# Kernel optimization log

Hardware: AMD Instinct MI355X
Metric: run time of the kernel (lower is better)

The kernel has to match this reference:

```python
import jax, jax.numpy as jnp
import numpy as np

R = 5            # num_relations
NEG_SLOPE = 0.2
N1 = 30000       # layer0 target count
N2 = 15000       # layer1 target count


def brgcn_conv(x_src, x_tgt, edge_index, edge_type, Wj, Wi, att_j, att_i,
               Wq, Wk, Wv, sw, sb, Wrel, heads, outc):
    """One BRGCNConv layer: per-relation GAT edge softmax + bilevel relation attention."""
    N = x_tgt.shape[0]
    hc = heads * outc
    hj = (x_src @ Wj).reshape(-1, heads, outc)   # [Ns,H,C]
    hi = (x_tgt @ Wi).reshape(-1, heads, outc)   # [N,H,C]
    src, tgt = edge_index[0], edge_index[1]
    xj = hj[src]                                  # [E,H,C]
    xi = hi[tgt]                                  # [E,H,C]
    # relation-specific attention logits per edge
    aj = jnp.sum(att_j[edge_type] * xj, axis=-1)  # [E,H]
    ai = jnp.sum(att_i[edge_type] * xi, axis=-1)  # [E,H]
    alpha = jax.nn.leaky_relu(aj + ai, NEG_SLOPE)
    # edge softmax grouped by (target node, relation) == per-relation propagate
    seg = tgt * R + edge_type                     # [E]
    nseg = N * R
    amax = jax.ops.segment_max(alpha, seg, num_segments=nseg)
    amax = jnp.where(jnp.isfinite(amax), amax, 0.0)
    ex = jnp.exp(alpha - amax[seg])
    den = jax.ops.segment_sum(ex, seg, num_segments=nseg)
    w = ex / jnp.maximum(den[seg], 1e-16)         # [E,H]
    msg = (w[:, :, None] * xj).reshape(-1, hc)    # [E,H*C]
    z = jax.ops.segment_sum(msg, seg, num_segments=nseg)
    z = z.reshape(N, R, hc).transpose(1, 0, 2)    # [R,N,H*C]; zero rows where no edges
    # per-relation Q/K/V
    q = jnp.einsum('rnd,rde->rne', z, Wq).reshape(R, N, heads, outc)
    k = jnp.einsum('rnd,rde->rne', z, Wk).reshape(R, N, heads, outc)
    v = jnp.einsum('rnd,rde->rne', z, Wv).reshape(R, N, heads, outc)
    # bilevel relation attention: psi[r,s,n,h] = <q_r, k_s>
    psi = jnp.einsum('rnhc,snhc->rsnh', q, k)
    mask = (psi == 0) & (jnp.sum(psi, axis=1, keepdims=True) != 0)
    prob = jax.nn.softmax(jnp.where(mask, -jnp.inf, psi), axis=1)
    delta = jnp.einsum('rsnh,snhc->rnhc', prob, v).reshape(R, N, hc)
    out = jnp.einsum('rnd,r->nd', delta, Wrel[:, 0])
    # single node type -> node_self[0] applied to every target node
    return out + x_tgt @ sw + sb


def setup_inputs() -> dict:
    key = jax.random.key(0)
    ks = jax.random.split(key, 32)
    H0, C0, H1, C1 = 4, 64, 1, 40
    IN, HC0 = 128, H0 * C0
    NG, N0 = 200000, 100000
    E0, E1 = 300000, 150000
    f = lambda k, s: jax.random.normal(k, s, dtype=jnp.float32) * 0.05
    return dict(
        n_id=jax.random.randint(ks[1], (N0,), 0, NG),
        local_node_idx=jax.random.randint(ks[2], (NG,), 0, NG),
        node_type=jnp.zeros((NG,), dtype=jnp.int32),
        edge_index0=jax.random.randint(ks[3], (2, E0), 0, N1),
        edge_type0=jax.random.randint(ks[4], (E0,), 0, R),
        edge_index1=jax.random.randint(ks[5], (2, E1), 0, N2),
        edge_type1=jax.random.randint(ks[6], (E1,), 0, R),
        emb=f(ks[0], (NG, IN)),
        Wj0=f(ks[7], (IN, HC0)), Wi0=f(ks[8], (IN, HC0)),
        att_j0=f(ks[9], (R, H0, C0)), att_i0=f(ks[10], (R, H0, C0)),
        Wq0=f(ks[11], (R, HC0, HC0)), Wk0=f(ks[12], (R, HC0, HC0)), Wv0=f(ks[13], (R, HC0, HC0)),
        sw0=f(ks[14], (IN, HC0)), sb0=f(ks[15], (HC0,)), Wrel0=f(ks[16], (R, 1)),
        Wj1=f(ks[17], (HC0, C1)), Wi1=f(ks[18], (HC0, C1)),
        att_j1=f(ks[19], (R, H1, C1)), att_i1=f(ks[20], (R, H1, C1)),
        Wq1=f(ks[21], (R, C1, C1)), Wk1=f(ks[22], (R, C1, C1)), Wv1=f(ks[23], (R, C1, C1)),
        sw1=f(ks[24], (HC0, C1)), sb1=f(ks[25], (C1,)), Wrel1=f(ks[26], (R, 1)),
    )


def reference(n_id, local_node_idx, node_type, edge_index0, edge_type0,
              edge_index1, edge_type1, emb,
              Wj0, Wi0, att_j0, att_i0, Wq0, Wk0, Wv0, sw0, sb0, Wrel0,
              Wj1, Wi1, att_j1, att_i1, Wq1, Wk1, Wv1, sw1, sb1, Wrel1):
    # group_input: single node type, all features from the embedding table
    x = emb[local_node_idx[n_id]]
    x1 = brgcn_conv(x, x[:N1], edge_index0, edge_type0, Wj0, Wi0, att_j0, att_i0,
                    Wq0, Wk0, Wv0, sw0, sb0, Wrel0, heads=4, outc=64)
    x1 = jax.nn.relu(x1)  # dropout p=0 in eval
    x2 = brgcn_conv(x1, x1[:N2], edge_index1, edge_type1, Wj1, Wi1, att_j1, att_i1,
                    Wq1, Wk1, Wv1, sw1, sb1, Wrel1, heads=1, outc=40)
    return jax.nn.log_softmax(x2, axis=-1)
```

## Files before the change

### kernel.cpp

```cpp
#include <hip/hip_runtime.h>
#include <hip/hip_bf16.h>

#define DI __device__ __forceinline__

DI float b2f(unsigned short u) {
    union { unsigned int i; float f; } x; x.i = ((unsigned int)u) << 16; return x.f;
}
DI unsigned short f2b(float f) {
    union { float f; unsigned int i; } x; x.f = f;
    unsigned int r = x.i + 0x7fff + ((x.i >> 16) & 1);
    return (unsigned short)(r >> 16);
}
DI float ldin(const void* p, long i, int f32) {
    return f32 ? ((const float*)p)[i] : b2f(((const unsigned short*)p)[i]);
}
DI void stval(float* p, float v) { *p = v; }
DI void stval(unsigned short* p, float v) { *p = f2b(v); }

static constexpr int N1 = 30000, N2 = 15000, R = 5;
static constexpr int IN = 128, HC0 = 256, C1 = 40;
static constexpr float NEGBIG = -1e30f;
static constexpr int LDK = 64;

typedef short bf16x8 __attribute__((ext_vector_type(8)));
typedef float f32x4 __attribute__((ext_vector_type(4)));

__global__ void detect_k(const void* emb, int* flag)
{
    int lane = threadIdx.x;
    int bad = 0;
    for (int j = 0; j < 4; ++j) {
        float f = b2f(((const unsigned short*)emb)[lane * 4 + j]);
        if (!(fabsf(f) < 1e8f)) bad = 1;
    }
    unsigned long long anybad = __ballot(bad != 0);
    if (lane == 0) *flag = (anybad != 0ull) ? 1 : 0;
}

struct PrepJobs {
    const void* src[12];
    unsigned short* dst[12];
    int K[12];
    int N[12];
    int per[12];
};
__global__ __launch_bounds__(256) void prep_all_k(
    PrepJobs J,
    const void* aj0, const void* ai0, const void* aj1, const void* ai1,
    unsigned short* A0j, unsigned short* A0i, unsigned short* A1j, unsigned short* A1i,
    int* __restrict__ cnt, int cntn,
    const int* __restrict__ dflag)
{
    const int f32 = *dflag;
    const int y = blockIdx.y;
    long t = (long)blockIdx.x * 256 + threadIdx.x;
    if (y < 12) {
        if (t >= J.per[y]) return;
        const int K = J.K[y], N = J.N[y];
        long kn = (long)K * N;
        long b = t / kn, rem = t % kn;
        long k = rem / N, n = rem % N;
        J.dst[y][(b * N + n) * K + k] = f2b(ldin(J.src[y], t, f32));
    } else {
        if (t < 20 * 256) {
            int j = (int)(t >> 8), k = (int)(t & 255);
            int h = j & 3, r = j >> 2;
            bool on = (k >> 6) == h;
            A0j[t] = f2b(on ? ldin(aj0, r * 256 + k, f32) : 0.f);
            A0i[t] = f2b(on ? ldin(ai0, r * 256 + k, f32) : 0.f);
        }
        if (t < 5 * 40) {
            A1j[t] = f2b(ldin(aj1, t, f32));
            A1i[t] = f2b(ldin(ai1, t, f32));
        }
        if (t < cntn) cnt[t] = 0;
    }
}

__global__ __launch_bounds__(256) void gather_k(
    const int* __restrict__ n_id, const int* __restrict__ lidx,
    const void* __restrict__ emb, unsigned short* __restrict__ x, int rows,
    const int* __restrict__ dflag)
{
    const int f32 = *dflag;
    long t = (long)blockIdx.x * 256 + threadIdx.x;
    long n = t >> 7, d = t & 127;
    if (n >= rows) return;
    long row = lidx[n_id[n]];
    x[n * IN + d] = f2b(ldin(emb, row * IN + d, f32));
}

DI void stage_fast(const unsigned short* __restrict__ G, int K,
                   unsigned short* S, int wave, int lane)
{
    const int p = lane >> 3;
    const int scol = ((lane & 7) ^ p) * 8;
#pragma unroll
    for (int t = 0; t < 4; ++t) {
        int row = t * 32 + wave * 8 + p;
        const unsigned short* src = G + (long)row * K + scol;
        unsigned short* dst = S + (t * 32 + wave * 8) * LDK;
        __builtin_amdgcn_global_load_lds(
            (const __attribute__((address_space(1))) unsigned int*)src,
            (__attribute__((address_space(3))) unsigned int*)dst, 16, 0, 0);
    }
}
DI void stage_slow(const unsigned short* __restrict__ G, int rows, int K,
                   int r0, int k0, unsigned short* S, int tid)
{
    const int sr = tid >> 1, sq = (tid & 1) * 32;
    const int sx = sr & 7;
    unsigned short* drow = S + sr * LDK;
    const unsigned short* g = G + (long)(r0 + sr) * K + k0 + sq;
    const bool rowok = (r0 + sr) < rows;
    const int s0 = sq >> 3;
    if (rowok && (k0 + sq + 32) <= K) {
        const uint4* gv = (const uint4*)g;
        uint4 a = gv[0], b = gv[1], c = gv[2], d = gv[3];
        *(uint4*)(drow + (((s0 + 0) ^ sx) << 3)) = a;
        *(uint4*)(drow + (((s0 + 1) ^ sx) << 3)) = b;
        *(uint4*)(drow + (((s0 + 2) ^ sx) << 3)) = c;
        *(uint4*)(drow + (((s0 + 3) ^ sx) << 3)) = d;
    } else if (!rowok) {
        uint4 zz = {0u, 0u, 0u, 0u};
        *(uint4*)(drow + (((s0 + 0) ^ sx) << 3)) = zz;
        *(uint4*)(drow + (((s0 + 1) ^ sx) << 3)) = zz;
        *(uint4*)(drow + (((s0 + 2) ^ sx) << 3)) = zz;
        *(uint4*)(drow + (((s0 + 3) ^ sx) << 3)) = zz;
    } else {
#pragma unroll 8
        for (int j = 0; j < 32; ++j) {
            int col = sq + j;
            int k = k0 + col;
            int widx = (((col >> 3) ^ sx) << 3) | (col & 7);
            drow[widx] = (k < K) ? g[j] : (unsigned short)0;
        }
    }
}

template <typename OT>
DI void gemm_mfma_body(
    const unsigned short* __restrict__ A, const unsigned short* __restrict__ Bt,
    OT* __restrict__ C, const void* __restrict__ bias, int f32,
    int M, int N, int K, unsigned short* As, unsigned short* Bs)
{
    const int tid = threadIdx.x;
    const int m0 = blockIdx.y * 128, n0 = blockIdx.x * 128;
    const int lane = tid & 63, wave = tid >> 6;
    const int wm = (wave & 1) * 64, wn = (wave >> 1) * 64;
    const int row16 = lane & 15, quad = lane >> 4;
    const bool kfull = (K & 63) == 0;
    const bool fastA = kfull && (m0 + 128 <= M);
    const bool fastB = kfull && (n0 + 128 <= N);
    f32x4 acc[4][4];
#pragma unroll
    for (int i = 0; i < 4; ++i)
#pragma unroll
        for (int j = 0; j < 4; ++j) acc[i][j] = {0.f, 0.f, 0.f, 0.f};

    for (int k0 = 0; k0 < K; k0 += 64) {
        if (fastA) stage_fast(A + (long)m0 * K + k0, K, As, wave, lane);
        else       stage_slow(A, M, K, m0, k0, As, tid);
        if (fastB) stage_fast(Bt + (long)n0 * K + k0, K, Bs, wave, lane);
        else       stage_slow(Bt, N, K, n0, k0, Bs, tid);
        __syncthreads();
#pragma unroll
        for (int ks = 0; ks < 64; ks += 32) {
            const int sw = (((quad + (ks >> 3)) ^ (row16 & 7)) << 3);
            bf16x8 af[4], bfr[4];
#pragma unroll
            for (int i = 0; i < 4; ++i)
                af[i] = *(const bf16x8*)(As + (wm + i * 16 + row16) * LDK + sw);
#pragma unroll
            for (int j = 0; j < 4; ++j)
                bfr[j] = *(const bf16x8*)(Bs + (wn + j * 16 + row16) * LDK + sw);
#pragma unroll
            for (int i = 0; i < 4; ++i)
#pragma unroll
                for (int j = 0; j < 4; ++j)
                    acc[i][j] = __builtin_amdgcn_mfma_f32_16x16x32_bf16(
                        af[i], bfr[j], acc[i][j], 0, 0, 0);
        }
        __syncthreads();
    }
#pragma unroll
    for (int i = 0; i < 4; ++i) {
#pragma unroll
        for (int reg = 0; reg < 4; ++reg) {
            const int gr = m0 + wm + i * 16 + quad * 4 + reg;
            if (gr >= M) continue;
#pragma unroll
            for (int j = 0; j < 4; ++j) {
                const int gc = n0 + wn + j * 16 + row16;
                if (gc >= N) continue;
                float v = acc[i][j][reg];
                if (bias) v += ldin(bias, gc, f32);
                stval(&C[(long)gr * N + gc], v);
            }
        }
    }
}

template <typename OT>
__global__ __launch_bounds__(256) void gemm_mfma3_k(
    const unsigned short* A0, const unsigned short* A1, const unsigned short* A2,
    const unsigned short* Bt0, const unsigned short* Bt1, const unsigned short* Bt2,
    OT* C0, OT* C1, OT* C2,
    const void* bias0, const void* bias1, const void* bias2,
    const int* __restrict__ dflag,
    int M, int N, int K, long sA, long sB, long sC, int nbatch)
{
    __shared__ unsigned short As[128 * LDK];
    __shared__ unsigned short Bs[128 * LDK];
    const int f32 = *dflag;
    const int sel = blockIdx.z / nbatch, b = blockIdx.z % nbatch;
    const unsigned short* A  = (sel == 0 ? A0 : sel == 1 ? A1 : A2) + (long)b * sA;
    const unsigned short* Bt = (sel == 0 ? Bt0 : sel == 1 ? Bt1 : Bt2) + (long)b * sB;
    OT* C = (sel == 0 ? C0 : sel == 1 ? C1 : C2) + (long)b * sC;
    const void* bias = sel == 0 ? bias0 : sel == 1 ? bias1 : bias2;
    gemm_mfma_body<OT>(A, Bt, C, bias, f32, M, N, K, As, Bs);
}

__global__ __launch_bounds__(256) void hist_k(const int* __restrict__ ei, int E, int* __restrict__ cnt)
{
    int e = blockIdx.x * 256 + threadIdx.x;
    if (e < E) atomicAdd(&cnt[ei[E + e]], 1);
}
__global__ __launch_bounds__(256) void scan1_k(
    const int* __restrict__ cnt, int* __restrict__ off, int* __restrict__ bsum, int n)
{
    __shared__ int buf[256];
    int i = blockIdx.x * 256 + threadIdx.x;
    int v = (i < n) ? cnt[i] : 0;
    buf[threadIdx.x] = v;
    __syncthreads();
#pragma unroll
    for (int s = 1; s < 256; s <<= 1) {
        int t = (threadIdx.x >= s) ? buf[threadIdx.x - s] : 0;
        __syncthreads();
        buf[threadIdx.x] += t;
        __syncthreads();
    }
    if (i < n) off[i] = buf[threadIdx.x] - v;
    if (threadIdx.x == 255) bsum[blockIdx.x] = buf[255];
}
__global__ void scan2_k(int* __restrict__ bsum, int nb, int* __restrict__ total_dst)
{
    __shared__ int buf[256];
    int v = (threadIdx.x < nb) ? bsum[threadIdx.x] : 0;
    buf[threadIdx.x] = v;
    __syncthreads();
#pragma unroll
    for (int s = 1; s < 256; s <<= 1) {
        int t = (threadIdx.x >= s) ? buf[threadIdx.x - s] : 0;
        __syncthreads();
        buf[threadIdx.x] += t;
        __syncthreads();
    }
    if (threadIdx.x < nb) bsum[threadIdx.x] = buf[threadIdx.x] - v;
    if (threadIdx.x == 255) *total_dst = buf[255];
}
__global__ __launch_bounds__(256) void scan3_k(
    int* __restrict__ off, int* __restrict__ cursor, const int* __restrict__ bsum,
    int* __restrict__ cnt, int n)
{
    int i = blockIdx.x * 256 + threadIdx.x;
    if (i < n) {
        int v = off[i] + bsum[blockIdx.x];
        off[i] = v;
        cursor[i] = v;
        cnt[i] = 0;
    }
}

__global__ __launch_bounds__(256) void scatter0_k(
    const int* __restrict__ ei, const int* __restrict__ et, int E,
    int* __restrict__ cursor,
    const float* __restrict__ ajn, const float* __restrict__ ain,
    int* __restrict__ src_s, int* __restrict__ rt_s, float* __restrict__ w4_s)
{
    int e = blockIdx.x * 256 + threadIdx.x;
    if (e >= E) return;
    int src = ei[e], tgt = ei[E + e], r = et[e];
    int p = atomicAdd(&cursor[tgt], 1);
    src_s[p] = src; rt_s[p] = r;
    float4 a = *(const float4*)(ajn + (long)src * 20 + r * 4);
    float4 b = *(const float4*)(ain + (long)tgt * 20 + r * 4);
    float4 w;
    float s0 = a.x + b.x, s1 = a.y + b.y, s2 = a.z + b.z, s3 = a.w + b.w;
    s0 = s0 > 0.f ? s0 : 0.2f * s0;  s1 = s1 > 0.f ? s1 : 0.2f * s1;
    s2 = s2 > 0.f ? s2 : 0.2f * s2;  s3 = s3 > 0.f ? s3 : 0.2f * s3;
    w.x = expf(fminf(s0, 60.f)); w.y = expf(fminf(s1, 60.f));
    w.z = expf(fminf(s2, 60.f)); w.w = expf(fminf(s3, 60.f));
    *(float4*)(w4_s + (long)p * 4) = w;
}
__global__ __launch_bounds__(256) void scatter1_k(
    const int* __restrict__ ei, const int* __restrict__ et, int E,
    int* __restrict__ cursor,
    const float* __restrict__ ajn, const float* __restrict__ ain,
    int* __restrict__ src_s, int* __restrict__ rt_s, float* __restrict__ w_s)
{
    int e = blockIdx.x * 256 + threadIdx.x;
    if (e >= E) return;
    int src = ei[e], tgt = ei[E + e], r = et[e];
    int p = atomicAdd(&cursor[tgt], 1);
    src_s[p] = src; rt_s[p] = r;
    float s = ajn[(long)src * 5 + r] + ain[(long)tgt * 5 + r];
    s = s > 0.f ? s : 0.2f * s;
    w_s[p] = expf(fminf(s, 60.f));
}

__global__ __launch_bounds__(256) void aggregate0_k(
    const int* __restrict__ src_s, const int* __restrict__ rt_s,
    const float* __restrict__ w4_s, const int* __restrict__ off,
    const unsigned short* __restrict__ hj,
    unsigned short* __restrict__ z, int Nn)
{
    int tgt = (int)((blockIdx.x * 256u + threadIdx.x) >> 6);
    int lane = threadIdx.x & 63;
    if (tgt >= Nn) return;
    int dd = lane * 4, h = lane >> 4;
    float acc[5][4] = {};
    float den[5] = {};
    int s = off[tgt], epd = off[tgt + 1];
    for (int i = s; i < epd; ++i) {
        int src = src_s[i];
        int r_e = rt_s[i];
        float wgt = w4_s[(long)i * 4 + h];
        ushort4 xj = *(const ushort4*)(hj + (long)src * 256 + dd);
        float x0 = b2f(xj.x), x1 = b2f(xj.y), x2 = b2f(xj.z), x3 = b2f(xj.w);
#pragma unroll
        for (int r = 0; r < 5; ++r) {
            float ws = (r == r_e) ? wgt : 0.f;
            den[r] += ws;
            acc[r][0] += ws * x0; acc[r][1] += ws * x1;
            acc[r][2] += ws * x2; acc[r][3] += ws * x3;
        }
    }
#pragma unroll
    for (int r = 0; r < 5; ++r) {
        float inv = 1.f / fmaxf(den[r], 1e-16f);
        ushort4 o;
        o.x = f2b(acc[r][0] * inv); o.y = f2b(acc[r][1] * inv);
        o.z = f2b(acc[r][2] * inv); o.w = f2b(acc[r][3] * inv);
        *(ushort4*)(z + ((long)r * Nn + tgt) * 256 + dd) = o;
    }
}

__global__ __launch_bounds__(256) void aggregate1_k(
    const int* __restrict__ src_s, const int* __restrict__ rt_s,
    const float* __restrict__ w_s, const int* __restrict__ off,
    const unsigned short* __restrict__ hj,
    unsigned short* __restrict__ z, int Nn)
{
    int tgt = (int)((blockIdx.x * 256u + threadIdx.x) >> 6);
    int lane = threadIdx.x & 63;
    if (tgt >= Nn) return;
    bool act = lane < 40;
    float acc[5] = {};
    float den[5] = {};
    int s = off[tgt], epd = off[tgt + 1];
    for (int i = s; i < epd; ++i) {
        int src = src_s[i];
        int r_e = rt_s[i];
        float wgt = w_s[i];
        float xj = act ? b2f(hj[(long)src * 40 + lane]) : 0.f;
#pragma unroll
        for (int r = 0; r < 5; ++r) {
            float ws = (r == r_e) ? wgt : 0.f;
            den[r] += ws;
            acc[r] += ws * xj;
        }
    }
    if (act) {
#pragma unroll
        for (int r = 0; r < 5; ++r) {
            float inv = 1.f / fmaxf(den[r], 1e-16f);
            z[((long)r * Nn + tgt) * 40 + lane] = f2b(acc[r] * inv);
        }
    }
}

__global__ __launch_bounds__(256) void fused_attn0_k(
    const unsigned short* __restrict__ qb, const unsigned short* __restrict__ kb,
    const unsigned short* __restrict__ vb, const void* __restrict__ wrel,
    unsigned short* __restrict__ x1, int n0, int nloc, int chq,
    const int* __restrict__ dflag)
{
    const int f32 = *dflag;
    int nl = (int)((blockIdx.x * 256u + threadIdx.x) >> 6);
    int lane = threadIdx.x & 63;
    if (nl >= nloc) return;
    int n = n0 + nl;
    int dd = lane * 4;
    float qf[5][4], kf[5][4];
#pragma unroll
    for (int r = 0; r < 5; ++r) {
        ushort4 qv = *(const ushort4*)(qb + ((long)r * chq + nl) * 256 + dd);
        ushort4 kv = *(const ushort4*)(kb + ((long)r * chq + nl) * 256 + dd);
        qf[r][0] = b2f(qv.x); qf[r][1] = b2f(qv.y); qf[r][2] = b2f(qv.z); qf[r][3] = b2f(qv.w);
        kf[r][0] = b2f(kv.x); kf[r][1] = b2f(kv.y); kf[r][2] = b2f(kv.z); kf[r][3] = b2f(kv.w);
    }
    float psi[5][5];
#pragma unroll
    for (int r = 0; r < 5; ++r)
#pragma unroll
        for (int s = 0; s < 5; ++s) {
            float p = qf[r][0] * kf[s][0] + qf[r][1] * kf[s][1] +
                      qf[r][2] * kf[s][2] + qf[r][3] * kf[s][3];
            p += __shfl_xor(p, 1, 64); p += __shfl_xor(p, 2, 64);
            p += __shfl_xor(p, 4, 64); p += __shfl_xor(p, 8, 64);
            psi[r][s] = p;
        }
    float pw[5] = {0.f, 0.f, 0.f, 0.f, 0.f};
#pragma unroll
    for (int r = 0; r < 5; ++r) {
        float rowsum = psi[r][0] + psi[r][1] + psi[r][2] + psi[r][3] + psi[r][4];
        float vals[5], m = NEGBIG;
#pragma unroll
        for (int s = 0; s < 5; ++s) {
            float v = (psi[r][s] == 0.f && rowsum != 0.f) ? NEGBIG : psi[r][s];
            vals[s] = v; m = fmaxf(m, v);
        }
        float es[5], sum = 0.f;
#pragma unroll
        for (int s = 0; s < 5; ++s) { es[s] = expf(vals[s] - m); sum += es[s]; }
        float wr = ldin(wrel, r, f32) / sum;
#pragma unroll
        for (int s = 0; s < 5; ++s) pw[s] += wr * es[s];
    }
    float acc[4] = {0.f, 0.f, 0.f, 0.f};
#pragma unroll
    for (int s = 0; s < 5; ++s) {
        ushort4 vv = *(const ushort4*)(vb + ((long)s * chq + nl) * 256 + dd);
        acc[0] += pw[s] * b2f(vv.x); acc[1] += pw[s] * b2f(vv.y);
        acc[2] += pw[s] * b2f(vv.z); acc[3] += pw[s] * b2f(vv.w);
    }
    ushort4* xp = (ushort4*)(x1 + (long)n * 256 + dd);
    ushort4 sv = *xp;
    sv.x = f2b(fmaxf(b2f(sv.x) + acc[0], 0.f));
    sv.y = f2b(fmaxf(b2f(sv.y) + acc[1], 0.f));
    sv.z = f2b(fmaxf(b2f(sv.z) + acc[2], 0.f));
    sv.w = f2b(fmaxf(b2f(sv.w) + acc[3], 0.f));
    *xp = sv;
}

__global__ __launch_bounds__(256) void fused_attn1_k(
    const unsigned short* __restrict__ qb, const unsigned short* __restrict__ kb,
    const unsigned short* __restrict__ vb, const void* __restrict__ wrel,
    const unsigned short* __restrict__ self1, void* __restrict__ out, int N,
    const int* __restrict__ dflag)
{
    const int f32 = *dflag;
    int n = (int)((blockIdx.x * 256u + threadIdx.x) >> 6);
    int lane = threadIdx.x & 63;
    if (n >= N) return;
    bool act = lane < 40;
    float qf[5], kf[5];
#pragma unroll
    for (int r = 0; r < 5; ++r) {
        long o = ((long)r * N + n) * 40 + lane;
        qf[r] = act ? b2f(qb[o]) : 0.f;
        kf[r] = act ? b2f(kb[o]) : 0.f;
    }
    float psi[5][5];
#pragma unroll
    for (int r = 0; r < 5; ++r)
#pragma unroll
        for (int s = 0; s < 5; ++s) {
            float p = qf[r] * kf[s];
            p += __shfl_xor(p, 1, 64);  p += __shfl_xor(p, 2, 64);
            p += __shfl_xor(p, 4, 64);  p += __shfl_xor(p, 8, 64);
            p += __shfl_xor(p, 16, 64); p += __shfl_xor(p, 32, 64);
            psi[r][s] = p;
        }
    float pw[5] = {0.f, 0.f, 0.f, 0.f, 0.f};
#pragma unroll
    for (int r = 0; r < 5; ++r) {
        float rowsum = psi[r][0] + psi[r][1] + psi[r][2] + psi[r][3] + psi[r][4];
        float vals[5], m = NEGBIG;
#pragma unroll
        for (int s = 0; s < 5; ++s) {
            float v = (psi[r][s] == 0.f && rowsum != 0.f) ? NEGBIG : psi[r][s];
            vals[s] = v; m = fmaxf(m, v);
        }
        float es[5], sum = 0.f;
#pragma unroll
        for (int s = 0; s < 5; ++s) { es[s] = expf(vals[s] - m); sum += es[s]; }
        float wr = ldin(wrel, r, f32) / sum;
#pragma unroll
        for (int s = 0; s < 5; ++s) pw[s] += wr * es[s];
    }
    float val = NEGBIG;
    if (act) {
        float acc = 0.f;
#pragma unroll
        for (int s = 0; s < 5; ++s) acc += pw[s] * b2f(vb[((long)s * N + n) * 40 + lane]);
        val = b2f(self1[(long)n * 40 + lane]) + acc;
    }
    float m = val;
#pragma unroll
    for (int msk = 1; msk < 64; msk <<= 1) m = fmaxf(m, __shfl_xor(m, msk, 64));
    float e = act ? expf(val - m) : 0.f;
#pragma unroll
    for (int msk = 1; msk < 64; msk <<= 1) e += __shfl_xor(e, msk, 64);
    if (act) {
        float r = val - m - logf(e);
        long oidx = (long)n * 40 + lane;
        if (f32) ((float*)out)[oidx] = r;
        else     ((unsigned short*)out)[oidx] = f2b(r);
    }
}

extern "C" void kernel_launch(void* const* d_in, const int* in_sizes, int n_in,
                              void* d_out, int out_size, void* d_ws, size_t ws_size,
                              hipStream_t stream)
{
    const int* n_id = (const int*)d_in[0];
    const int* lidx = (const int*)d_in[1];
    const int* ei0  = (const int*)d_in[3];
    const int* et0  = (const int*)d_in[4];
    const int* ei1  = (const int*)d_in[5];
    const int* et1  = (const int*)d_in[6];
    const void* emb = d_in[7];
    const void* Wj0 = d_in[8];  const void* Wi0 = d_in[9];
    const void* aj0 = d_in[10]; const void* ai0 = d_in[11];
    const void* Wq0 = d_in[12]; const void* Wk0 = d_in[13]; const void* Wv0 = d_in[14];
    const void* sw0 = d_in[15]; const void* sb0 = d_in[16]; const void* Wr0 = d_in[17];
    const void* Wj1 = d_in[18]; const void* Wi1 = d_in[19];
    const void* aj1 = d_in[20]; const void* ai1 = d_in[21];
    const void* Wq1 = d_in[22]; const void* Wk1 = d_in[23]; const void* Wv1 = d_in[24];
    const void* sw1 = d_in[25]; const void* sb1 = d_in[26]; const void* Wr1 = d_in[27];
    const int E0 = in_sizes[4], E1 = in_sizes[6];

    auto al = [](size_t b) { return (b + 255) & ~(size_t)255; };

    const size_t P_total =
        al((size_t)R * N1 * HC0 * 2) +
        al((size_t)N1 * HC0 * 2) +
        2 * al((size_t)N1 * 20 * 4) +
        3 * al((size_t)(N1 + 1) * 4) +
        al(256 * 4) +
        2 * al((size_t)E0 * 4) +
        al((size_t)E0 * 16) +
        3 * al((size_t)HC0 * IN * 2) +
        3 * al((size_t)R * HC0 * HC0 * 2) +
        3 * al((size_t)C1 * HC0 * 2) +
        3 * al((size_t)R * C1 * C1 * 2) +
        2 * al(20 * 256 * 2) + 2 * al(5 * 40 * 2) +
        al(256);

    int CH = 15000;
    {
        size_t need = 3 * al((size_t)R * CH * HC0 * 2) + P_total + (16u << 20);
        if (need > ws_size) CH = 7500;
    }
    const size_t QB = al((size_t)R * CH * HC0 * 2);

    char* w = (char*)d_ws;
    unsigned short* qc = (unsigned short*)(w);
    unsigned short* kc = (unsigned short*)(w + QB);
    unsigned short* vc = (unsigned short*)(w + 2 * QB);
    unsigned short* x30k = (unsigned short*)(w);
    unsigned short* hj0  = (unsigned short*)(w + al((size_t)N1 * IN * 2));
    unsigned short* hi0  = (unsigned short*)((char*)hj0 + al((size_t)N1 * HC0 * 2));
    size_t o1 = 0;
    auto take1 = [&](size_t b) { char* p = w + o1; o1 += (b + 255) & ~(size_t)255; return p; };
    unsigned short* hj1   = (unsigned short*)take1((size_t)N2 * C1 * 2);
    unsigned short* hi1   = (unsigned short*)take1((size_t)N2 * C1 * 2);
    unsigned short* self1 = (unsigned short*)take1((size_t)N2 * C1 * 2);
    float* ajn1 = (float*)take1((size_t)N2 * R * 4);
    float* ain1 = (float*)take1((size_t)N2 * R * 4);
    unsigned short* z1  = (unsigned short*)take1((size_t)R * N2 * C1 * 2);
    unsigned short* q1b = (unsigned short*)take1((size_t)R * N2 * C1 * 2);
    unsigned short* k1b = (unsigned short*)take1((size_t)R * N2 * C1 * 2);
    unsigned short* v1b = (unsigned short*)take1((size_t)R * N2 * C1 * 2);
    size_t o = 3 * QB;
    auto take = [&](size_t b) { char* p = w + o; o += (b + 255) & ~(size_t)255; return p; };
    unsigned short* z0 = (unsigned short*)take((size_t)R * N1 * HC0 * 2);
    unsigned short* x1 = (unsigned short*)take((size_t)N1 * HC0 * 2);
    float* ajn0 = (float*)take((size_t)N1 * 20 * 4);
    float* ain0 = (float*)take((size_t)N1 * 20 * 4);
    int* cnt    = (int*)take((size_t)(N1 + 1) * 4);
    int* off    = (int*)take((size_t)(N1 + 1) * 4);
    int* cursor = (int*)take((size_t)(N1 + 1) * 4);
    int* bsum   = (int*)take(256 * 4);
    int* src_s  = (int*)take((size_t)E0 * 4);
    int* rt_s   = (int*)take((size_t)E0 * 4);
    float* w4_s = (float*)take((size_t)E0 * 16);
    unsigned short* wjt0 = (unsigned short*)take((size_t)HC0 * IN * 2);
    unsigned short* wit0 = (unsigned short*)take((size_t)HC0 * IN * 2);
    unsigned short* swt0 = (unsigned short*)take((size_t)HC0 * IN * 2);
    unsigned short* wqt0 = (unsigned short*)take((size_t)R * HC0 * HC0 * 2);
    unsigned short* wkt0 = (unsigned short*)take((size_t)R * HC0 * HC0 * 2);
    unsigned short* wvt0 = (unsigned short*)take((size_t)R * HC0 * HC0 * 2);
    unsigned short* wjt1 = (unsigned short*)take((size_t)C1 * HC0 * 2);
    unsigned short* wit1 = (unsigned short*)take((size_t)C1 * HC0 * 2);
    unsigned short* swt1 = (unsigned short*)take((size_t)C1 * HC0 * 2);
    unsigned short* wqt1 = (unsigned short*)take((size_t)R * C1 * C1 * 2);
    unsigned short* wkt1 = (unsigned short*)take((size_t)R * C1 * C1 * 2);
    unsigned short* wvt1 = (unsigned short*)take((size_t)R * C1 * C1 * 2);
    unsigned short* atA0j = (unsigned short*)take(20 * 256 * 2);
    unsigned short* atA0i = (unsigned short*)take(20 * 256 * 2);
    unsigned short* atA1j = (unsigned short*)take(5 * 40 * 2);
    unsigned short* atA1i = (unsigned short*)take(5 * 40 * 2);
    int* dflag = (int*)take(256);

    detect_k<<<1, 64, 0, stream>>>(emb, dflag);

    {
        PrepJobs J;
        const void* srcs[12] = {Wj0, Wi0, sw0, Wq0, Wk0, Wv0, Wj1, Wi1, sw1, Wq1, Wk1, Wv1};
        unsigned short* dsts[12] = {wjt0, wit0, swt0, wqt0, wkt0, wvt0,
                                    wjt1, wit1, swt1, wqt1, wkt1, wvt1};
        int Ks[12] = {IN, IN, IN, HC0, HC0, HC0, HC0, HC0, HC0, C1, C1, C1};
        int Ns[12] = {HC0, HC0, HC0, HC0, HC0, HC0, C1, C1, C1, C1, C1, C1};
        int pers[12] = {IN * HC0, IN * HC0, IN * HC0,
                        R * HC0 * HC0, R * HC0 * HC0, R * HC0 * HC0,
                        HC0 * C1, HC0 * C1, HC0 * C1,
                        R * C1 * C1, R * C1 * C1, R * C1 * C1};
        for (int i = 0; i < 12; ++i) {
            J.src[i] = srcs[i]; J.dst[i] = dsts[i];
            J.K[i] = Ks[i]; J.N[i] = Ns[i]; J.per[i] = pers[i];
        }
        int xb = (R * HC0 * HC0 + 255) / 256;
        prep_all_k<<<dim3((unsigned)xb, 13), 256, 0, stream>>>(
            J, aj0, ai0, aj1, ai1, atA0j, atA0i, atA1j, atA1i, cnt, N1 + 1, dflag);
    }

    gather_k<<<(int)(((long)N1 * IN + 255) / 256), 256, 0, stream>>>(n_id, lidx, emb, x30k, N1, dflag);
    gemm_mfma3_k<unsigned short><<<dim3(2, (N1 + 127) / 128, 3), 256, 0, stream>>>(
        x30k, x30k, x30k, wjt0, wit0, swt0, hj0, hi0, x1, nullptr, nullptr, sb0,
        dflag, N1, HC0, IN, 0, 0, 0, 1);
    gemm_mfma3_k<float><<<dim3(1, (N1 + 127) / 128, 2), 256, 0, stream>>>(
        hj0, hi0, hi0, atA0j, atA0i, atA0i, ajn0, ain0, ain0, nullptr, nullptr, nullptr,
        dflag, N1, 20, HC0, 0, 0, 0, 1);

    hist_k<<<(E0 + 255) / 256, 256, 0, stream>>>(ei0, E0, cnt);
    {
        int nb = (N1 + 255) / 256;
        scan1_k<<<nb, 256, 0, stream>>>(cnt, off, bsum, N1);
        scan2_k<<<1, 256, 0, stream>>>(bsum, nb, off + N1);
        scan3_k<<<nb, 256, 0, stream>>>(off, cursor, bsum, cnt, N1);
    }
    scatter0_k<<<(E0 + 255) / 256, 256, 0, stream>>>(ei0, et0, E0, cursor, ajn0, ain0, src_s, rt_s, w4_s);
    aggregate0_k<<<(N1 + 3) / 4, 256, 0, stream>>>(src_s, rt_s, w4_s, off, hj0, z0, N1);

    {
        const int nch = N1 / CH;
        const long sA = (long)N1 * HC0, sB = (long)HC0 * HC0, sC = (long)CH * HC0;
        for (int c = 0; c < nch; ++c) {
            const unsigned short* zc = z0 + (long)c * CH * HC0;
            gemm_mfma3_k<unsigned short><<<dim3(2, (CH + 127) / 128, 3 * R), 256, 0, stream>>>(
                zc, zc, zc, wqt0, wkt0, wvt0, qc, kc, vc, nullptr, nullptr, nullptr,
                dflag, CH, HC0, HC0, sA, sB, sC, R);
            fused_attn0_k<<<(CH + 3) / 4, 256, 0, stream>>>(qc, kc, vc, Wr0, x1, c * CH, CH, CH, dflag);
        }
    }

    gemm_mfma3_k<unsigned short><<<dim3(1, (N2 + 127) / 128, 3), 256, 0, stream>>>(
        x1, x1, x1, wjt1, wit1, swt1, hj1, hi1, self1, nullptr, nullptr, sb1,
        dflag, N2, C1, HC0, 0, 0, 0, 1);
    gemm_mfma3_k<float><<<dim3(1, (N2 + 127) / 128, 2), 256, 0, stream>>>(
        hj1, hi1, hi1, atA1j, atA1i, atA1i, ajn1, ain1, ain1, nullptr, nullptr, nullptr,
        dflag, N2, 5, C1, 0, 0, 0, 1);

    hist_k<<<(E1 + 255) / 256, 256, 0, stream>>>(ei1, E1, cnt);
    {
        int nb = (N2 + 255) / 256;
        scan1_k<<<nb, 256, 0, stream>>>(cnt, off, bsum, N2);
        scan2_k<<<1, 256, 0, stream>>>(bsum, nb, off + N2);
        scan3_k<<<nb, 256, 0, stream>>>(off, cursor, bsum, cnt, N2);
    }
    scatter1_k<<<(E1 + 255) / 256, 256, 0, stream>>>(ei1, et1, E1, cursor, ajn1, ain1, src_s, rt_s, w4_s);
    aggregate1_k<<<(N2 + 3) / 4, 256, 0, stream>>>(src_s, rt_s, w4_s, off, hj1, z1, N2);

    {
        long sA = (long)N2 * C1, sB = (long)C1 * C1, sC = (long)N2 * C1;
        gemm_mfma3_k<unsigned short><<<dim3(1, (N2 + 127) / 128, 3 * R), 256, 0, stream>>>(
            z1, z1, z1, wqt1, wkt1, wvt1, q1b, k1b, v1b, nullptr, nullptr, nullptr,
            dflag, N2, C1, C1, sA, sB, sC, R);
    }
    fused_attn1_k<<<(N2 + 3) / 4, 256, 0, stream>>>(q1b, k1b, v1b, Wr1, self1, d_out, N2, dflag);
}
```

Before: 664.0 us.

## Add A-resident GEMM that reuses one LDS A tile across three weight matrices

Adds a GEMM kernel that loads the full-K A tile (128 rows) into LDS once. It then loops over the three B matrices (Wj/Wi/self, or Q/K/V per relation), staging only B per K step. This replaces launches in which each of the three outputs was a separate z-slice that reloaded A from global memory. The kernel uses up to about 80KB of LDS per block, which lowers occupancy. The A staging has no row bounds check on the last partial tile.

```diff
diff --git a/kernel.cpp b/kernel.cpp
--- a/kernel.cpp
+++ b/kernel.cpp
@@ -89,6 +89,7 @@
     long row = lidx[n_id[n]];
     x[n * IN + d] = f2b(ldin(emb, row * IN + d, f32));
 }
+
 
 DI void stage_fast(const unsigned short* __restrict__ G, int K,
                    unsigned short* S, int wave, int lane)
@@ -134,6 +135,109 @@
             int k = k0 + col;
             int widx = (((col >> 3) ^ sx) << 3) | (col & 7);
             drow[widx] = (k < K) ? g[j] : (unsigned short)0;
+        }
+    }
+}
+
+DI void stageA(const unsigned short* __restrict__ G, int K,
+               unsigned short* S, int wave, int lane)
+{
+    if (K == 256) {
+        const int lrow = lane >> 5, slin = lane & 31;
+#pragma unroll
+        for (int t = 0; t < 16; ++t) {
+            int rbase = wave * 32 + t * 2;
+            int row = rbase + lrow;
+            const unsigned short* src = G + (long)row * 256 + ((slin ^ (row & 7)) << 3);
+            unsigned short* dst = S + rbase * 256;
+            __builtin_amdgcn_global_load_lds(
+                (const __attribute__((address_space(1))) unsigned int*)src,
+                (__attribute__((address_space(3))) unsigned int*)dst, 16, 0, 0);
+        }
+    } else {
+        const int lrow = lane >> 4, slin = lane & 15;
+#pragma unroll
+        for (int t = 0; t < 8; ++t) {
+            int rbase = wave * 32 + t * 4;
+            int row = rbase + lrow;
+            const unsigned short* src = G + (long)row * 128 + ((slin ^ (row & 7)) << 3);
+            unsigned short* dst = S + rbase * 128;
+            __builtin_amdgcn_global_load_lds(
+                (const __attribute__((address_space(1))) unsigned int*)src,
+                (__attribute__((address_space(3))) unsigned int*)dst, 16, 0, 0);
+        }
+    }
+}
+
+__global__ __launch_bounds__(256) void gemm_ares_k(
+    const unsigned short* __restrict__ Ab,
+    const unsigned short* B0, const unsigned short* B1, const unsigned short* B2,
+    unsigned short* C0, unsigned short* C1, unsigned short* C2,
+    const void* bias0, const void* bias1, const void* bias2,
+    const int* __restrict__ dflag,
+    int M, int K, long sA, long sB, long sC)
+{
+    __shared__ unsigned short As[128 * 256];
+    __shared__ unsigned short Bs[128 * LDK];
+    const int f32 = *dflag;
+    const int tid = threadIdx.x;
+    const int lane = tid & 63, wave = tid >> 6;
+    const int b = blockIdx.z;
+    const int n0 = blockIdx.x * 128, m0 = blockIdx.y * 128;
+    const int wm = (wave & 1) * 64, wn = (wave >> 1) * 64;
+    const int row16 = lane & 15, quad = lane >> 4;
+
+    stageA(Ab + (long)b * sA + (long)m0 * K, K, As, wave, lane);
+
+#pragma unroll 1
+    for (int sel = 0; sel < 3; ++sel) {
+        const unsigned short* Bt = (sel == 0 ? B0 : sel == 1 ? B1 : B2)
+                                   + (long)b * sB + (long)n0 * K;
+        unsigned short* C = (sel == 0 ? C0 : sel == 1 ? C1 : C2) + (long)b * sC;
+        const void* bias = sel == 0 ? bias0 : sel == 1 ? bias1 : bias2;
+        f32x4 acc[4][4];
+#pragma unroll
+        for (int i = 0; i < 4; ++i)
+#pragma unroll
+            for (int j = 0; j < 4; ++j) acc[i][j] = {0.f, 0.f, 0.f, 0.f};
+
+        for (int k0 = 0; k0 < K; k0 += 64) {
+            stage_fast(Bt + k0, K, Bs, wave, lane);
+            __syncthreads();
+#pragma unroll
+            for (int ks = 0; ks < 64; ks += 32) {
+                const int saw = ((((k0 + ks) >> 3) + quad) ^ (row16 & 7)) << 3;
+                const int sbw = (((quad + (ks >> 3)) ^ (row16 & 7)) << 3);
+                bf16x8 af[4], bfr[4];
+#pragma unroll
+                for (int i = 0; i < 4; ++i)
+                    af[i] = *(const bf16x8*)(As + (wm + i * 16 + row16) * K + saw);
+#pragma unroll
+                for (int j = 0; j < 4; ++j)
+                    bfr[j] = *(const bf16x8*)(Bs + (wn + j * 16 + row16) * LDK + sbw);
+#pragma unroll
+                for (int i = 0; i < 4; ++i)
+#pragma unroll
+                    for (int j = 0; j < 4; ++j)
+                        acc[i][j] = __builtin_amdgcn_mfma_f32_16x16x32_bf16(
+                            af[i], bfr[j], acc[i][j], 0, 0, 0);
+            }
+            __syncthreads();
+        }
+#pragma unroll
+        for (int i = 0; i < 4; ++i) {
+#pragma unroll
+            for (int reg = 0; reg < 4; ++reg) {
+                const int gr = m0 + wm + i * 16 + quad * 4 + reg;
+                if (gr >= M) continue;
+#pragma unroll
+                for (int j = 0; j < 4; ++j) {
+                    const int gc = n0 + wn + j * 16 + row16;
+                    float v = acc[i][j][reg];
+                    if (bias) v += ldin(bias, gc, f32);
+                    C[(long)gr * 256 + gc] = f2b(v);
+                }
+            }
         }
     }
 }
@@ -629,9 +733,9 @@
     }
 
     gather_k<<<(int)(((long)N1 * IN + 255) / 256), 256, 0, stream>>>(n_id, lidx, emb, x30k, N1, dflag);
-    gemm_mfma3_k<unsigned short><<<dim3(2, (N1 + 127) / 128, 3), 256, 0, stream>>>(
-        x30k, x30k, x30k, wjt0, wit0, swt0, hj0, hi0, x1, nullptr, nullptr, sb0,
-        dflag, N1, HC0, IN, 0, 0, 0, 1);
+    gemm_ares_k<<<dim3(2, (N1 + 127) / 128, 1), 256, 0, stream>>>(
+        x30k, wjt0, wit0, swt0, hj0, hi0, x1, nullptr, nullptr, sb0,
+        dflag, N1, IN, 0, 0, 0);
     gemm_mfma3_k<float><<<dim3(1, (N1 + 127) / 128, 2), 256, 0, stream>>>(
         hj0, hi0, hi0, atA0j, atA0i, atA0i, ajn0, ain0, ain0, nullptr, nullptr, nullptr,
         dflag, N1, 20, HC0, 0, 0, 0, 1);
@@ -648,12 +752,11 @@
 
     {
         const int nch = N1 / CH;
-        const long sA = (long)N1 * HC0, sB = (long)HC0 * HC0, sC = (long)CH * HC0;
         for (int c = 0; c < nch; ++c) {
             const unsigned short* zc = z0 + (long)c * CH * HC0;
-            gemm_mfma3_k<unsigned short><<<dim3(2, (CH + 127) / 128, 3 * R), 256, 0, stream>>>(
-                zc, zc, zc, wqt0, wkt0, wvt0, qc, kc, vc, nullptr, nullptr, nullptr,
-                dflag, CH, HC0, HC0, sA, sB, sC, R);
+            gemm_ares_k<<<dim3(2, (CH + 127) / 128, R), 256, 0, stream>>>(
+                zc, wqt0, wkt0, wvt0, qc, kc, vc, nullptr, nullptr, nullptr,
+                dflag, CH, HC0, (long)N1 * HC0, (long)HC0 * HC0, (long)CH * HC0);
             fused_attn0_k<<<(CH + 3) / 4, 256, 0, stream>>>(qc, kc, vc, Wr0, x1, c * CH, CH, CH, dflag);
         }
     }
```

Result: no change. 657.3 us (-1.0%).
